# Kernel optimization log

Measured on AMD Instinct MI355X. Metric: run time of the kernel, lower is better.

The kernel has to match this reference:

```python
import jax, jax.numpy as jnp
import numpy as np

C = 256
EPS = 1e-5

def layer_norm(x, g, b):
    mu = jnp.mean(x, axis=-1, keepdims=True)
    var = jnp.var(x, axis=-1, keepdims=True)
    return (x - mu) * jax.lax.rsqrt(var + EPS) * g + b

def setup_inputs() -> dict:
    key = jax.random.key(0)
    ks = jax.random.split(key, 12)
    B, H, W = 1, 64, 64
    s = 1.0 / np.sqrt(C)
    inp = {
        'lidar_features': jax.random.normal(ks[0], (B, C, H, W), jnp.float32),
        'image_features': jax.random.normal(ks[1], (B, C, H, W), jnp.float32),
        'Wq': jax.random.normal(ks[2], (C, C), jnp.float32) * s,
        'bq': jnp.zeros((C,), jnp.float32),
        'Wk': jax.random.normal(ks[3], (C, C), jnp.float32) * s,
        'bk': jnp.zeros((C,), jnp.float32),
        'Wv': jax.random.normal(ks[4], (C, C), jnp.float32) * s,
        'bv': jnp.zeros((C,), jnp.float32),
        'Wo': jax.random.normal(ks[5], (C, C), jnp.float32) * s,
        'bo': jnp.zeros((C,), jnp.float32),
        'g1': jnp.ones((C,), jnp.float32),
        'b1': jnp.zeros((C,), jnp.float32),
        'W1': jax.random.normal(ks[6], (C, 4 * C), jnp.float32) * s,
        'bf1': jnp.zeros((4 * C,), jnp.float32),
        'W2': jax.random.normal(ks[7], (4 * C, C), jnp.float32) * (1.0 / np.sqrt(4 * C)),
        'bf2': jnp.zeros((C,), jnp.float32),
        'g2': jnp.ones((C,), jnp.float32),
        'b2': jnp.zeros((C,), jnp.float32),
        'num_heads': 8,
    }
    return inp

def reference(lidar_features, image_features, Wq, bq, Wk, bk, Wv, bv, Wo, bo,
              g1, b1, W1, bf1, W2, bf2, g2, b2, num_heads):
    B, Cc, H, W = lidar_features.shape
    S = H * W
    hd = Cc // num_heads
    # [B,C,H,W] -> [B,S,C]
    x = lidar_features.reshape(B, Cc, S).transpose(0, 2, 1)
    y = image_features.reshape(B, Cc, S).transpose(0, 2, 1)
    q = x @ Wq + bq            # [B,S,C]
    k = y @ Wk + bk
    v = y @ Wv + bv
    qh = q.reshape(B, S, num_heads, hd).transpose(0, 2, 1, 3)  # [B,h,S,d]
    kh = k.reshape(B, S, num_heads, hd).transpose(0, 2, 1, 3)
    vh = v.reshape(B, S, num_heads, hd).transpose(0, 2, 1, 3)
    attn = jnp.einsum('bhqd,bhkd->bhqk', qh, kh) / jnp.sqrt(jnp.float32(hd))
    attn = jax.nn.softmax(attn, axis=-1)
    out = jnp.einsum('bhqk,bhkd->bhqd', attn, vh)
    out = out.transpose(0, 2, 1, 3).reshape(B, S, Cc)
    out = out @ Wo + bo
    # residual is the projected q in [B,S,C] layout (intended semantics)
    out = layer_norm(q + out, g1, b1)
    ffn = jax.nn.relu(out @ W1 + bf1) @ W2 + bf2
    out = layer_norm(out + ffn, g2, b2)
    return out.reshape(B, H, W, Cc).transpose(0, 3, 1, 2)
```

## Files before the change

### kernel.cpp

```cpp
#include <hip/hip_runtime.h>

#define SQ 4096
#define CCH 256
#define NH 8
#define HD 32
#define LN_EPS 1e-5f
#define NSPLIT 8

typedef __bf16 bf16x8 __attribute__((ext_vector_type(8)));
typedef float f32x4 __attribute__((ext_vector_type(4)));
using bf16 = __bf16;

#define LOG2E 1.4426950408889634f

__device__ __forceinline__ void tile_tc(const float* __restrict__ src, bf16* __restrict__ dst,
                                        int R, int Ccol, int ti, int tj) {
    __shared__ float t[32][33];
    const int tx = threadIdx.x & 31;
    const int ty = threadIdx.x >> 5;
    const int i0 = ti * 32, j0 = tj * 32;
    #pragma unroll
    for (int i = 0; i < 32; i += 8)
        t[ty + i][tx] = src[(size_t)(i0 + ty + i) * Ccol + j0 + tx];
    __syncthreads();
    #pragma unroll
    for (int i = 0; i < 32; i += 8)
        dst[(size_t)(j0 + ty + i) * R + i0 + tx] = (bf16)t[tx][ty + i];
}

__global__ __launch_bounds__(256)
void cvt_inputs(const float* __restrict__ x, const float* __restrict__ y,
                bf16* __restrict__ xT, bf16* __restrict__ yT) {
    const float* s = blockIdx.z ? y : x;
    bf16* d = blockIdx.z ? yT : xT;
    tile_tc(s, d, CCH, SQ, blockIdx.y, blockIdx.x);
}

__global__ __launch_bounds__(256)
void cvt_weights(const float* Wq, const float* Wk, const float* Wv, const float* Wo,
                 const float* W1, const float* W2,
                 bf16* WqT, bf16* WkT, bf16* WvT, bf16* WoT, bf16* W1T, bf16* W2T) {
    const int id = blockIdx.x;
    if (id < 256) {
        const int w = id >> 6, local = id & 63;
        const float* s = (w == 0) ? Wq : (w == 1) ? Wk : (w == 2) ? Wv : Wo;
        bf16* d = (w == 0) ? WqT : (w == 1) ? WkT : (w == 2) ? WvT : WoT;
        tile_tc(s, d, 256, 256, local >> 3, local & 7);
    } else if (id < 512) {
        const int local = id - 256;
        tile_tc(W1, W1T, 256, 1024, local >> 5, local & 31);
    } else {
        const int local = id - 512;
        tile_tc(W2, W2T, 1024, 256, local >> 3, local & 7);
    }
}

template <int K, int OUT_MODE, bool RELU>
__global__ __launch_bounds__(256)
void gemm_mfma(const bf16* __restrict__ A, const bf16* __restrict__ BT,
               const float* __restrict__ bias, float* __restrict__ Cf,
               bf16* __restrict__ Cb, int N, float bscale) {
    const int tid = threadIdx.x;
    const int w = tid >> 6, l = tid & 63;
    const int l15 = l & 15, lg = l >> 4;
    const int m0 = blockIdx.x * 64 + (w >> 1) * 32;
    const int n0 = blockIdx.y * 64 + (w & 1) * 32;

    f32x4 acc[2][2] = {};
    const bf16* a0 = &A[(size_t)(m0 + l15) * K + lg * 8];
    const bf16* b0 = &BT[(size_t)(n0 + l15) * K + lg * 8];

    for (int k0 = 0; k0 < K; k0 += 32) {
        bf16x8 a[2], b[2];
        a[0] = *reinterpret_cast<const bf16x8*>(a0 + k0);
        a[1] = *reinterpret_cast<const bf16x8*>(a0 + (size_t)16 * K + k0);
        b[0] = *reinterpret_cast<const bf16x8*>(b0 + k0);
        b[1] = *reinterpret_cast<const bf16x8*>(b0 + (size_t)16 * K + k0);
        #pragma unroll
        for (int i = 0; i < 2; ++i)
            #pragma unroll
            for (int j = 0; j < 2; ++j)
                acc[i][j] = __builtin_amdgcn_mfma_f32_16x16x32_bf16(a[i], b[j], acc[i][j], 0, 0, 0);
    }

    #pragma unroll
    for (int i = 0; i < 2; ++i) {
        #pragma unroll
        for (int j = 0; j < 2; ++j) {
            const int col = n0 + j * 16 + l15;
            const float bs = bias[col];
            #pragma unroll
            for (int r = 0; r < 4; ++r) {
                const int row = m0 + i * 16 + lg * 4 + r;
                float val = acc[i][j][r] + bs;
                if (RELU) val = fmaxf(val, 0.f);
                if constexpr (OUT_MODE == 0)
                    Cf[(size_t)row * N + col] = val;
                if constexpr (OUT_MODE == 2)
                    Cb[(size_t)row * N + col] = (bf16)(val * bscale);
            }
        }
    }
}

__global__ __launch_bounds__(256)
void qkv_gemm(const bf16* __restrict__ xT, const bf16* __restrict__ yT,
              const bf16* __restrict__ WqT, const bf16* __restrict__ WkT,
              const bf16* __restrict__ WvT,
              const float* __restrict__ bq, const float* __restrict__ bk,
              const float* __restrict__ bv,
              bf16* __restrict__ qb, bf16* __restrict__ kbb, bf16* __restrict__ vTb,
              float kscale) {
    const int z = blockIdx.z;
    const bf16* A  = (z == 0) ? xT : yT;
    const bf16* BT = (z == 0) ? WqT : (z == 1) ? WkT : WvT;
    const float* bias = (z == 0) ? bq : (z == 1) ? bk : bv;

    const int tid = threadIdx.x;
    const int w = tid >> 6, l = tid & 63;
    const int l15 = l & 15, lg = l >> 4;
    const int m0 = blockIdx.x * 64 + (w >> 1) * 32;
    const int n0 = blockIdx.y * 64 + (w & 1) * 32;

    f32x4 acc[2][2] = {};
    const bf16* a0 = &A[(size_t)(m0 + l15) * CCH + lg * 8];
    const bf16* b0 = &BT[(size_t)(n0 + l15) * CCH + lg * 8];

    for (int k0 = 0; k0 < CCH; k0 += 32) {
        bf16x8 a[2], b[2];
        a[0] = *reinterpret_cast<const bf16x8*>(a0 + k0);
        a[1] = *reinterpret_cast<const bf16x8*>(a0 + (size_t)16 * CCH + k0);
        b[0] = *reinterpret_cast<const bf16x8*>(b0 + k0);
        b[1] = *reinterpret_cast<const bf16x8*>(b0 + (size_t)16 * CCH + k0);
        #pragma unroll
        for (int i = 0; i < 2; ++i)
            #pragma unroll
            for (int j = 0; j < 2; ++j)
                acc[i][j] = __builtin_amdgcn_mfma_f32_16x16x32_bf16(a[i], b[j], acc[i][j], 0, 0, 0);
    }

    const float sc = (z == 1) ? kscale : 1.f;
    #pragma unroll
    for (int i = 0; i < 2; ++i) {
        #pragma unroll
        for (int j = 0; j < 2; ++j) {
            const int col = n0 + j * 16 + l15;
            const float bs = bias[col];
            #pragma unroll
            for (int r = 0; r < 4; ++r) {
                const int row = m0 + i * 16 + lg * 4 + r;
                float val = acc[i][j][r] + bs;
                if (z == 2)
                    vTb[(size_t)col * SQ + row] = (bf16)val;
                else if (z == 1)
                    kbb[(size_t)row * CCH + col] = (bf16)(val * sc);
                else
                    qb[(size_t)row * CCH + col] = (bf16)val;
            }
        }
    }
}

__global__ __launch_bounds__(256)
void flash_attn9(const bf16* __restrict__ qb, const bf16* __restrict__ kb,
                 const bf16* __restrict__ vT, bf16* __restrict__ Op,
                 float* __restrict__ Lp) {
    const int fid = blockIdx.x + 16 * (blockIdx.y + NH * blockIdx.z);
    const int nid = (fid & 7) * 128 + (fid >> 3);
    const int q0 = (nid & 15) * 256;
    const int h  = (nid >> 4) & 7;
    const int sp = nid >> 7;

    const int tid = threadIdx.x;
    const int w = tid >> 6, l = tid & 63;
    const int l15 = l & 15, lg = l >> 4;

    __shared__ unsigned int Sb[4][2][8][72];

    bf16x8 aq[4];
    #pragma unroll
    for (int su = 0; su < 4; ++su)
        aq[su] = *reinterpret_cast<const bf16x8*>(
            &qb[(size_t)(q0 + su * 64 + w * 16 + l15) * CCH + h * HD + lg * 8]);

    float lac[4] = {0.f, 0.f, 0.f, 0.f};
    f32x4 o[4][2] = {};

    const bf16* kfrag = &kb[(size_t)l15 * CCH + h * HD + lg * 8];
    const bf16* vfrag = &vT[(size_t)(h * HD + l15) * SQ + lg * 8];

    const int kt0 = sp * (SQ / NSPLIT / 64);
    const int kt1 = kt0 + (SQ / NSPLIT / 64);

    for (int kt = kt0; kt < kt1; ++kt) {
        const int kb0 = kt * 64;

        bf16x8 kf[4], vf[2][2];
        #pragma unroll
        for (int t = 0; t < 4; ++t)
            kf[t] = *reinterpret_cast<const bf16x8*>(kfrag + (size_t)(kb0 + t * 16) * CCH);
        #pragma unroll
        for (int dh = 0; dh < 2; ++dh)
            #pragma unroll
            for (int kh = 0; kh < 2; ++kh)
                vf[dh][kh] = *reinterpret_cast<const bf16x8*>(
                    vfrag + (size_t)dh * 16 * SQ + kb0 + kh * 32);

        #pragma unroll
        for (int su = 0; su < 4; ++su) {
            const int par = su & 1;
            f32x4 s[4];
            #pragma unroll
            for (int t = 0; t < 4; ++t)
                s[t] = __builtin_amdgcn_mfma_f32_16x16x32_bf16(
                    kf[t], aq[su], (f32x4){0.f, 0.f, 0.f, 0.f}, 0, 0, 0);

            #pragma unroll
            for (int t = 0; t < 4; ++t) {
                float p0 = exp2f(s[t][0]), p1 = exp2f(s[t][1]);
                float p2 = exp2f(s[t][2]), p3 = exp2f(s[t][3]);
                lac[su] += (p0 + p1) + (p2 + p3);
                unsigned int u0 = __builtin_bit_cast(unsigned int, p0) + 0x8000u;
                unsigned int u1 = __builtin_bit_cast(unsigned int, p1) + 0x8000u;
                unsigned int u2 = __builtin_bit_cast(unsigned int, p2) + 0x8000u;
                unsigned int u3 = __builtin_bit_cast(unsigned int, p3) + 0x8000u;
                Sb[w][par][t * 2 + 0][l] = __builtin_amdgcn_perm(u1, u0, 0x07060302u);
                Sb[w][par][t * 2 + 1][l] = __builtin_amdgcn_perm(u3, u2, 0x07060302u);
            }

            #pragma unroll
            for (int kh = 0; kh < 2; ++kh) {
                const int sbase = kh * 4 + (lg >> 1) * 2;
                const int i0 = l15 + 16 * ((lg & 1) * 2);
                const int i1 = i0 + 16;
                union { unsigned int u[4]; bf16x8 v; } pb;
                pb.u[0] = Sb[w][par][sbase + 0][i0];
                pb.u[1] = Sb[w][par][sbase + 1][i0];
                pb.u[2] = Sb[w][par][sbase + 0][i1];
                pb.u[3] = Sb[w][par][sbase + 1][i1];
                #pragma unroll
                for (int dh = 0; dh < 2; ++dh)
                    o[su][dh] = __builtin_amdgcn_mfma_f32_16x16x32_bf16(
                        vf[dh][kh], pb.v, o[su][dh], 0, 0, 0);
            }
        }
    }

    const size_t obase = ((size_t)sp * NH + h) * HD;
    #pragma unroll
    for (int su = 0; su < 4; ++su) {
        float lx = lac[su];
        lx += __shfl_xor(lx, 16);
        lx += __shfl_xor(lx, 32);
        const int qrow = q0 + su * 64 + w * 16 + l15;
        #pragma unroll
        for (int dh = 0; dh < 2; ++dh)
            #pragma unroll
            for (int r = 0; r < 4; ++r)
                Op[(obase + dh * 16 + lg * 4 + r) * SQ + qrow] = (bf16)o[su][dh][r];
        if (lg == 0)
            Lp[((size_t)sp * NH + h) * SQ + qrow] = lx;
    }
}

__global__ __launch_bounds__(256)
void attn_merge3(const bf16* __restrict__ Op, const float* __restrict__ Lp,
                 bf16* __restrict__ atb) {
    const int h = blockIdx.y;
    const int q0 = blockIdx.x * 64;
    const int t = threadIdx.x;
    __shared__ float sInv[64];
    __shared__ float trans[32][65];

    if (t < 64) {
        float L = 0.f;
        #pragma unroll
        for (int sp = 0; sp < NSPLIT; ++sp)
            L += Lp[((size_t)sp * NH + h) * SQ + q0 + t];
        sInv[t] = 1.0f / L;
    }
    __syncthreads();

    const int q = t & 63, dg = t >> 6;
    float a[8] = {0.f, 0.f, 0.f, 0.f, 0.f, 0.f, 0.f, 0.f};
    for (int sp = 0; sp < NSPLIT; ++sp) {
        const size_t rb = ((size_t)sp * NH + h) * HD;
        #pragma unroll
        for (int i = 0; i < 8; ++i) {
            const int d = i * 4 + dg;
            a[i] += (float)Op[(rb + d) * SQ + q0 + q];
        }
    }
    const float invq = sInv[q];
    #pragma unroll
    for (int i = 0; i < 8; ++i)
        trans[i * 4 + dg][q] = a[i] * invq;
    __syncthreads();

    const int oq = t >> 2, od = (t & 3) * 8;
    bf16x8 o8;
    #pragma unroll
    for (int j = 0; j < 8; ++j) o8[j] = (bf16)trans[od + j][oq];
    *reinterpret_cast<bf16x8*>(&atb[(size_t)(q0 + oq) * CCH + h * HD + od]) = o8;
}

__global__ __launch_bounds__(256)
void add_ln1(const bf16* __restrict__ a, const float* __restrict__ b,
             const float* __restrict__ g, const float* __restrict__ beta,
             float* __restrict__ out, bf16* __restrict__ outb) {
    const int s = blockIdx.x;
    const int c = threadIdx.x;
    float val = (float)a[(size_t)s * CCH + c] + b[(size_t)s * CCH + c];
    float sum = val, sq = val * val;
    #pragma unroll
    for (int off = 1; off < 64; off <<= 1) {
        sum += __shfl_xor(sum, off);
        sq  += __shfl_xor(sq, off);
    }
    __shared__ float ssum[4], ssq[4];
    int w = c >> 6;
    if ((c & 63) == 0) { ssum[w] = sum; ssq[w] = sq; }
    __syncthreads();
    sum = ssum[0] + ssum[1] + ssum[2] + ssum[3];
    sq  = ssq[0] + ssq[1] + ssq[2] + ssq[3];
    float mu = sum * (1.0f / CCH);
    float var = sq * (1.0f / CCH) - mu * mu;
    float rs = rsqrtf(var + LN_EPS);
    float res = (val - mu) * rs * g[c] + beta[c];
    out[(size_t)s * CCH + c] = res;
    outb[(size_t)s * CCH + c] = (bf16)res;
}

__global__ __launch_bounds__(256)
void add_ln_t(const float* __restrict__ a, const float* __restrict__ b,
              const float* __restrict__ g, const float* __restrict__ beta,
              float* __restrict__ out) {
    const int s0 = blockIdx.x * 32;
    const int t = threadIdx.x;
    const int row = t >> 3;
    const int e8 = t & 7;
    const size_t base = (size_t)(s0 + row) * CCH + e8 * 32;

    float v[32];
    float sum = 0.f, sq = 0.f;
    #pragma unroll
    for (int j = 0; j < 32; j += 4) {
        float4 va = *reinterpret_cast<const float4*>(&a[base + j]);
        float4 vb = *reinterpret_cast<const float4*>(&b[base + j]);
        v[j]     = va.x + vb.x;
        v[j + 1] = va.y + vb.y;
        v[j + 2] = va.z + vb.z;
        v[j + 3] = va.w + vb.w;
        sum += (v[j] + v[j + 1]) + (v[j + 2] + v[j + 3]);
        sq  += (v[j] * v[j] + v[j + 1] * v[j + 1]) + (v[j + 2] * v[j + 2] + v[j + 3] * v[j + 3]);
    }
    sum += __shfl_xor(sum, 1); sum += __shfl_xor(sum, 2); sum += __shfl_xor(sum, 4);
    sq  += __shfl_xor(sq, 1);  sq  += __shfl_xor(sq, 2);  sq  += __shfl_xor(sq, 4);
    const float mu = sum * (1.0f / CCH);
    const float var = sq * (1.0f / CCH) - mu * mu;
    const float rs = rsqrtf(var + LN_EPS);
    #pragma unroll
    for (int j = 0; j < 32; j += 4) {
        float4 gg = *reinterpret_cast<const float4*>(&g[e8 * 32 + j]);
        float4 bb = *reinterpret_cast<const float4*>(&beta[e8 * 32 + j]);
        v[j]     = (v[j]     - mu) * rs * gg.x + bb.x;
        v[j + 1] = (v[j + 1] - mu) * rs * gg.y + bb.y;
        v[j + 2] = (v[j + 2] - mu) * rs * gg.z + bb.z;
        v[j + 3] = (v[j + 3] - mu) * rs * gg.w + bb.w;
    }

    __shared__ float tile[32][33];
    const int cl = t >> 3, f4 = (t & 7) * 4;
    for (int c = 0; c < 8; ++c) {
        __syncthreads();
        if (e8 == c) {
            #pragma unroll
            for (int j = 0; j < 32; ++j) tile[j][row] = v[j];
        }
        __syncthreads();
        float4 o4 = {tile[cl][f4], tile[cl][f4 + 1], tile[cl][f4 + 2], tile[cl][f4 + 3]};
        *reinterpret_cast<float4*>(&out[(size_t)(c * 32 + cl) * SQ + s0 + f4]) = o4;
    }
}

extern "C" void kernel_launch(void* const* d_in, const int* in_sizes, int n_in,
                              void* d_out, int out_size, void* d_ws, size_t ws_size,
                              hipStream_t stream) {
    const float* lidar = (const float*)d_in[0];
    const float* image = (const float*)d_in[1];
    const float* Wq  = (const float*)d_in[2];
    const float* bq  = (const float*)d_in[3];
    const float* Wk  = (const float*)d_in[4];
    const float* bk  = (const float*)d_in[5];
    const float* Wv  = (const float*)d_in[6];
    const float* bv  = (const float*)d_in[7];
    const float* Wo  = (const float*)d_in[8];
    const float* bo  = (const float*)d_in[9];
    const float* g1  = (const float*)d_in[10];
    const float* b1  = (const float*)d_in[11];
    const float* W1  = (const float*)d_in[12];
    const float* bf1 = (const float*)d_in[13];
    const float* W2  = (const float*)d_in[14];
    const float* bf2 = (const float*)d_in[15];
    const float* g2  = (const float*)d_in[16];
    const float* b2  = (const float*)d_in[17];
    float* out = (float*)d_out;

    char* ws = (char*)d_ws;
    const size_t KB = 1024, MBy = 1024 * 1024;
    bf16* qb   = (bf16*)(ws + 0);
    bf16* kbb  = (bf16*)(ws + 2 * MBy);
    bf16* vTb  = (bf16*)(ws + 4 * MBy);
    bf16* WoT  = (bf16*)(ws + 6 * MBy);
    bf16* W1T  = (bf16*)(ws + 6 * MBy + 128 * KB);
    bf16* W2T  = (bf16*)(ws + 6 * MBy + 640 * KB);
    bf16* WqT  = (bf16*)(ws + 6 * MBy + 1152 * KB);
    bf16* WkT  = (bf16*)(ws + 6 * MBy + 1280 * KB);
    bf16* WvT  = (bf16*)(ws + 6 * MBy + 1408 * KB);
    bf16* xT   = (bf16*)(ws + 7 * MBy + 512 * KB);
    bf16* yT   = (bf16*)(ws + 9 * MBy + 512 * KB);
    bf16* Op   = (bf16*)(ws + 7 * MBy + 512 * KB);
    float* Lp  = (float*)d_out;
    bf16* atb  = (bf16*)(ws + 2 * MBy);
    float* o   = (float*)(ws + 7 * MBy + 512 * KB);
    float* ln1 = (float*)(ws + 11 * MBy + 512 * KB);
    bf16* ln1b = (bf16*)(ws + 4 * MBy);
    bf16* h1   = (bf16*)(ws + 15 * MBy + 512 * KB);
    float* h2  = (float*)(ws + 7 * MBy + 512 * KB);

    const float qscale = 0.17677669529663687f * 1.4426950408889634f;
    dim3 blk(256);

    cvt_inputs<<<dim3(SQ / 32, CCH / 32, 2), blk, 0, stream>>>(lidar, image, xT, yT);
    cvt_weights<<<dim3(768), blk, 0, stream>>>(Wq, Wk, Wv, Wo, W1, W2,
                                               WqT, WkT, WvT, WoT, W1T, W2T);
    qkv_gemm<<<dim3(64, 4, 3), blk, 0, stream>>>(xT, yT, WqT, WkT, WvT,
                                                 bq, bk, bv, qb, kbb, vTb, qscale);
    flash_attn9<<<dim3(SQ / 256, NH, NSPLIT), blk, 0, stream>>>(qb, kbb, vTb, Op, Lp);
    attn_merge3<<<dim3(SQ / 64, NH), blk, 0, stream>>>(Op, Lp, atb);
    gemm_mfma<256, 0, false><<<dim3(64, 4), blk, 0, stream>>>(atb, WoT, bo, o, nullptr, 256, 1.f);
    add_ln1<<<SQ, blk, 0, stream>>>(qb, o, g1, b1, ln1, ln1b);
    gemm_mfma<256, 2, true ><<<dim3(64, 16), blk, 0, stream>>>(ln1b, W1T, bf1, nullptr, h1, 1024, 1.f);
    gemm_mfma<1024, 0, false><<<dim3(64, 4), blk, 0, stream>>>(h1, W2T, bf2, h2, nullptr, 256, 1.f);
    add_ln_t<<<dim3(SQ / 32), blk, 0, stream>>>(ln1, h2, g2, b2, out);
}
```

Baseline: 141.3 us.

## Compute softmax row sums via ones-row MFMA, halve attention splits, split-K output GEMMs

The V-transpose buffer is padded with 16 extra rows per head, one of them all ones, so an extra MFMA yields the softmax denominator and replaces the scalar per-lane sum accumulation. Rounding before bf16 packing is dropped. Attention KV splits drop from 8 to 4, giving longer loops per block and fewer partials to merge. The Wo and W2 GEMMs become split-K with two partial outputs that the layernorm kernels add together, which doubles block count for these small GEMMs at the cost of extra memory traffic. The workspace layout is reshuffled to fit the larger buffers.

```diff
diff --git a/kernel.cpp b/kernel.cpp
--- a/kernel.cpp
+++ b/kernel.cpp
@@ -5,13 +5,12 @@
 #define NH 8
 #define HD 32
 #define LN_EPS 1e-5f
-#define NSPLIT 8
+#define NSPLIT 4
+#define VROWS 48
 
 typedef __bf16 bf16x8 __attribute__((ext_vector_type(8)));
 typedef float f32x4 __attribute__((ext_vector_type(4)));
 using bf16 = __bf16;
-
-#define LOG2E 1.4426950408889634f
 
 __device__ __forceinline__ void tile_tc(const float* __restrict__ src, bf16* __restrict__ dst,
                                         int R, int Ccol, int ti, int tj) {
@@ -39,7 +38,8 @@
 __global__ __launch_bounds__(256)
 void cvt_weights(const float* Wq, const float* Wk, const float* Wv, const float* Wo,
                  const float* W1, const float* W2,
-                 bf16* WqT, bf16* WkT, bf16* WvT, bf16* WoT, bf16* W1T, bf16* W2T) {
+                 bf16* WqT, bf16* WkT, bf16* WvT, bf16* WoT, bf16* W1T, bf16* W2T,
+                 bf16* vTb) {
     const int id = blockIdx.x;
     if (id < 256) {
         const int w = id >> 6, local = id & 63;
@@ -49,9 +49,23 @@
     } else if (id < 512) {
         const int local = id - 256;
         tile_tc(W1, W1T, 256, 1024, local >> 5, local & 31);
-    } else {
+    } else if (id < 768) {
         const int local = id - 512;
         tile_tc(W2, W2T, 1024, 256, local >> 3, local & 7);
+    } else {
+        const int local = id - 768;
+        #pragma unroll
+        for (int rr = 0; rr < 2; ++rr) {
+            const int pr = local * 2 + rr;
+            const int hh = pr >> 4, j = pr & 15;
+            const bf16 val = (bf16)((j == 0) ? 1.0f : 0.0f);
+            bf16x8 v8;
+            #pragma unroll
+            for (int e = 0; e < 8; ++e) v8[e] = val;
+            bf16* dst = vTb + ((size_t)hh * VROWS + 32 + j) * SQ + threadIdx.x * 16;
+            *reinterpret_cast<bf16x8*>(dst) = v8;
+            *reinterpret_cast<bf16x8*>(dst + 8) = v8;
+        }
     }
 }
 
@@ -59,7 +73,7 @@
 __global__ __launch_bounds__(256)
 void gemm_mfma(const bf16* __restrict__ A, const bf16* __restrict__ BT,
                const float* __restrict__ bias, float* __restrict__ Cf,
-               bf16* __restrict__ Cb, int N, float bscale) {
+               bf16* __restrict__ Cb, int N) {
     const int tid = threadIdx.x;
     const int w = tid >> 6, l = tid & 63;
     const int l15 = l & 15, lg = l >> 4;
@@ -97,7 +111,52 @@
                 if constexpr (OUT_MODE == 0)
                     Cf[(size_t)row * N + col] = val;
                 if constexpr (OUT_MODE == 2)
-                    Cb[(size_t)row * N + col] = (bf16)(val * bscale);
+                    Cb[(size_t)row * N + col] = (bf16)val;
+            }
+        }
+    }
+}
+
+template <int K, int KS>
+__global__ __launch_bounds__(256)
+void gemm_sk(const bf16* __restrict__ A, const bf16* __restrict__ BT,
+             const float* __restrict__ bias, float* __restrict__ Cf, int N) {
+    constexpr int KSL = K / KS;
+    const int z = blockIdx.z;
+    const int tid = threadIdx.x;
+    const int w = tid >> 6, l = tid & 63;
+    const int l15 = l & 15, lg = l >> 4;
+    const int m0 = blockIdx.x * 64 + (w >> 1) * 32;
+    const int n0 = blockIdx.y * 64 + (w & 1) * 32;
+
+    f32x4 acc[2][2] = {};
+    const bf16* a0 = &A[(size_t)(m0 + l15) * K + z * KSL + lg * 8];
+    const bf16* b0 = &BT[(size_t)(n0 + l15) * K + z * KSL + lg * 8];
+
+    for (int k0 = 0; k0 < KSL; k0 += 32) {
+        bf16x8 a[2], b[2];
+        a[0] = *reinterpret_cast<const bf16x8*>(a0 + k0);
+        a[1] = *reinterpret_cast<const bf16x8*>(a0 + (size_t)16 * K + k0);
+        b[0] = *reinterpret_cast<const bf16x8*>(b0 + k0);
+        b[1] = *reinterpret_cast<const bf16x8*>(b0 + (size_t)16 * K + k0);
+        #pragma unroll
+        for (int i = 0; i < 2; ++i)
+            #pragma unroll
+            for (int j = 0; j < 2; ++j)
+                acc[i][j] = __builtin_amdgcn_mfma_f32_16x16x32_bf16(a[i], b[j], acc[i][j], 0, 0, 0);
+    }
+
+    float* C = Cf + (size_t)z * SQ * N;
+    #pragma unroll
+    for (int i = 0; i < 2; ++i) {
+        #pragma unroll
+        for (int j = 0; j < 2; ++j) {
+            const int col = n0 + j * 16 + l15;
+            const float bs = (z == 0) ? bias[col] : 0.f;
+            #pragma unroll
+            for (int r = 0; r < 4; ++r) {
+                const int row = m0 + i * 16 + lg * 4 + r;
+                C[(size_t)row * N + col] = acc[i][j][r] + bs;
             }
         }
     }
@@ -151,7 +210,7 @@
                 const int row = m0 + i * 16 + lg * 4 + r;
                 float val = acc[i][j][r] + bs;
                 if (z == 2)
-                    vTb[(size_t)col * SQ + row] = (bf16)val;
+                    vTb[((size_t)(col >> 5) * VROWS + (col & 31)) * SQ + row] = (bf16)val;
                 else if (z == 1)
                     kbb[(size_t)row * CCH + col] = (bf16)(val * sc);
                 else
@@ -162,11 +221,11 @@
 }
 
 __global__ __launch_bounds__(256)
-void flash_attn9(const bf16* __restrict__ qb, const bf16* __restrict__ kb,
-                 const bf16* __restrict__ vT, bf16* __restrict__ Op,
-                 float* __restrict__ Lp) {
+void flash_attn10(const bf16* __restrict__ qb, const bf16* __restrict__ kb,
+                  const bf16* __restrict__ vT, bf16* __restrict__ Op,
+                  float* __restrict__ Lp) {
     const int fid = blockIdx.x + 16 * (blockIdx.y + NH * blockIdx.z);
-    const int nid = (fid & 7) * 128 + (fid >> 3);
+    const int nid = (fid & 7) * 64 + (fid >> 3);
     const int q0 = (nid & 15) * 256;
     const int h  = (nid >> 4) & 7;
     const int sp = nid >> 7;
@@ -183,11 +242,11 @@
         aq[su] = *reinterpret_cast<const bf16x8*>(
             &qb[(size_t)(q0 + su * 64 + w * 16 + l15) * CCH + h * HD + lg * 8]);
 
-    float lac[4] = {0.f, 0.f, 0.f, 0.f};
     f32x4 o[4][2] = {};
+    f32x4 o2[4] = {};
 
     const bf16* kfrag = &kb[(size_t)l15 * CCH + h * HD + lg * 8];
-    const bf16* vfrag = &vT[(size_t)(h * HD + l15) * SQ + lg * 8];
+    const bf16* vfrag = &vT[((size_t)h * VROWS + l15) * SQ + lg * 8];
 
     const int kt0 = sp * (SQ / NSPLIT / 64);
     const int kt1 = kt0 + (SQ / NSPLIT / 64);
@@ -195,12 +254,12 @@
     for (int kt = kt0; kt < kt1; ++kt) {
         const int kb0 = kt * 64;
 
-        bf16x8 kf[4], vf[2][2];
+        bf16x8 kf[4], vf[3][2];
         #pragma unroll
         for (int t = 0; t < 4; ++t)
             kf[t] = *reinterpret_cast<const bf16x8*>(kfrag + (size_t)(kb0 + t * 16) * CCH);
         #pragma unroll
-        for (int dh = 0; dh < 2; ++dh)
+        for (int dh = 0; dh < 3; ++dh)
             #pragma unroll
             for (int kh = 0; kh < 2; ++kh)
                 vf[dh][kh] = *reinterpret_cast<const bf16x8*>(
@@ -217,13 +276,10 @@
 
             #pragma unroll
             for (int t = 0; t < 4; ++t) {
-                float p0 = exp2f(s[t][0]), p1 = exp2f(s[t][1]);
-                float p2 = exp2f(s[t][2]), p3 = exp2f(s[t][3]);
-                lac[su] += (p0 + p1) + (p2 + p3);
-                unsigned int u0 = __builtin_bit_cast(unsigned int, p0) + 0x8000u;
-                unsigned int u1 = __builtin_bit_cast(unsigned int, p1) + 0x8000u;
-                unsigned int u2 = __builtin_bit_cast(unsigned int, p2) + 0x8000u;
-                unsigned int u3 = __builtin_bit_cast(unsigned int, p3) + 0x8000u;
+                unsigned int u0 = __builtin_bit_cast(unsigned int, exp2f(s[t][0]));
+                unsigned int u1 = __builtin_bit_cast(unsigned int, exp2f(s[t][1]));
+                unsigned int u2 = __builtin_bit_cast(unsigned int, exp2f(s[t][2]));
+                unsigned int u3 = __builtin_bit_cast(unsigned int, exp2f(s[t][3]));
                 Sb[w][par][t * 2 + 0][l] = __builtin_amdgcn_perm(u1, u0, 0x07060302u);
                 Sb[w][par][t * 2 + 1][l] = __builtin_amdgcn_perm(u3, u2, 0x07060302u);
             }
@@ -242,6 +298,8 @@
                 for (int dh = 0; dh < 2; ++dh)
                     o[su][dh] = __builtin_amdgcn_mfma_f32_16x16x32_bf16(
                         vf[dh][kh], pb.v, o[su][dh], 0, 0, 0);
+                o2[su] = __builtin_amdgcn_mfma_f32_16x16x32_bf16(
+                    vf[2][kh], pb.v, o2[su], 0, 0, 0);
             }
         }
     }
@@ -249,9 +307,6 @@
     const size_t obase = ((size_t)sp * NH + h) * HD;
     #pragma unroll
     for (int su = 0; su < 4; ++su) {
-        float lx = lac[su];
-        lx += __shfl_xor(lx, 16);
-        lx += __shfl_xor(lx, 32);
         const int qrow = q0 + su * 64 + w * 16 + l15;
         #pragma unroll
         for (int dh = 0; dh < 2; ++dh)
@@ -259,7 +314,7 @@
             for (int r = 0; r < 4; ++r)
                 Op[(obase + dh * 16 + lg * 4 + r) * SQ + qrow] = (bf16)o[su][dh][r];
         if (lg == 0)
-            Lp[((size_t)sp * NH + h) * SQ + qrow] = lx;
+            Lp[((size_t)sp * NH + h) * SQ + qrow] = o2[su][0];
     }
 }
 
@@ -310,7 +365,8 @@
              float* __restrict__ out, bf16* __restrict__ outb) {
     const int s = blockIdx.x;
     const int c = threadIdx.x;
-    float val = (float)a[(size_t)s * CCH + c] + b[(size_t)s * CCH + c];
+    const size_t idx = (size_t)s * CCH + c;
+    float val = (float)a[idx] + b[idx] + b[idx + (size_t)SQ * CCH];
     float sum = val, sq = val * val;
     #pragma unroll
     for (int off = 1; off < 64; off <<= 1) {
@@ -327,8 +383,8 @@
     float var = sq * (1.0f / CCH) - mu * mu;
     float rs = rsqrtf(var + LN_EPS);
     float res = (val - mu) * rs * g[c] + beta[c];
-    out[(size_t)s * CCH + c] = res;
-    outb[(size_t)s * CCH + c] = (bf16)res;
+    out[idx] = res;
+    outb[idx] = (bf16)res;
 }
 
 __global__ __launch_bounds__(256)
@@ -340,6 +396,7 @@
     const int row = t >> 3;
     const int e8 = t & 7;
     const size_t base = (size_t)(s0 + row) * CCH + e8 * 32;
+    const size_t PS = (size_t)SQ * CCH;
 
     float v[32];
     float sum = 0.f, sq = 0.f;
@@ -347,10 +404,11 @@
     for (int j = 0; j < 32; j += 4) {
         float4 va = *reinterpret_cast<const float4*>(&a[base + j]);
         float4 vb = *reinterpret_cast<const float4*>(&b[base + j]);
-        v[j]     = va.x + vb.x;
-        v[j + 1] = va.y + vb.y;
-        v[j + 2] = va.z + vb.z;
-        v[j + 3] = va.w + vb.w;
+        float4 vc = *reinterpret_cast<const float4*>(&b[base + PS + j]);
+        v[j]     = va.x + vb.x + vc.x;
+        v[j + 1] = va.y + vb.y + vc.y;
+        v[j + 2] = va.z + vb.z + vc.z;
+        v[j + 3] = va.w + vb.w + vc.w;
         sum += (v[j] + v[j + 1]) + (v[j + 2] + v[j + 3]);
         sq  += (v[j] * v[j] + v[j + 1] * v[j + 1]) + (v[j + 2] * v[j + 2] + v[j + 3] * v[j + 3]);
     }
@@ -407,40 +465,40 @@
     float* out = (float*)d_out;
 
     char* ws = (char*)d_ws;
-    const size_t KB = 1024, MBy = 1024 * 1024;
-    bf16* qb   = (bf16*)(ws + 0);
-    bf16* kbb  = (bf16*)(ws + 2 * MBy);
-    bf16* vTb  = (bf16*)(ws + 4 * MBy);
-    bf16* WoT  = (bf16*)(ws + 6 * MBy);
-    bf16* W1T  = (bf16*)(ws + 6 * MBy + 128 * KB);
-    bf16* W2T  = (bf16*)(ws + 6 * MBy + 640 * KB);
-    bf16* WqT  = (bf16*)(ws + 6 * MBy + 1152 * KB);
-    bf16* WkT  = (bf16*)(ws + 6 * MBy + 1280 * KB);
-    bf16* WvT  = (bf16*)(ws + 6 * MBy + 1408 * KB);
-    bf16* xT   = (bf16*)(ws + 7 * MBy + 512 * KB);
-    bf16* yT   = (bf16*)(ws + 9 * MBy + 512 * KB);
-    bf16* Op   = (bf16*)(ws + 7 * MBy + 512 * KB);
-    float* Lp  = (float*)d_out;
-    bf16* atb  = (bf16*)(ws + 2 * MBy);
-    float* o   = (float*)(ws + 7 * MBy + 512 * KB);
-    float* ln1 = (float*)(ws + 11 * MBy + 512 * KB);
-    bf16* ln1b = (bf16*)(ws + 4 * MBy);
-    bf16* h1   = (bf16*)(ws + 15 * MBy + 512 * KB);
-    float* h2  = (float*)(ws + 7 * MBy + 512 * KB);
+    const size_t KB = 1024;
+    bf16* W2T = (bf16*)(ws + 0);
+    bf16* W1T = (bf16*)(ws + 512 * KB);
+    bf16* WoT = (bf16*)(ws + 1024 * KB);
+    bf16* WqT = (bf16*)(ws + 1152 * KB);
+    bf16* WkT = (bf16*)(ws + 1280 * KB);
+    bf16* WvT = (bf16*)(ws + 1408 * KB);
+    bf16* qb  = (bf16*)(ws + 1536 * KB);
+    bf16* kbb = (bf16*)(ws + 3584 * KB);
+    bf16* vTb = (bf16*)(ws + 5632 * KB);
+    bf16* xT  = (bf16*)(ws + 8704 * KB);
+    bf16* yT  = (bf16*)(ws + 10752 * KB);
+    bf16* Op  = (bf16*)(ws + 8704 * KB);
+    float* Lp = (float*)d_out;
+    bf16* atb = (bf16*)(ws + 3584 * KB);
+    float* o01 = (float*)(ws + 8704 * KB);
+    float* ln1 = (float*)(ws + 19968 * KB);
+    bf16* ln1b = (bf16*)(ws + 5632 * KB);
+    bf16* h1  = (bf16*)(ws + 9728 * KB);
+    float* h2 = (float*)(ws + 1536 * KB);
 
     const float qscale = 0.17677669529663687f * 1.4426950408889634f;
     dim3 blk(256);
 
     cvt_inputs<<<dim3(SQ / 32, CCH / 32, 2), blk, 0, stream>>>(lidar, image, xT, yT);
-    cvt_weights<<<dim3(768), blk, 0, stream>>>(Wq, Wk, Wv, Wo, W1, W2,
-                                               WqT, WkT, WvT, WoT, W1T, W2T);
+    cvt_weights<<<dim3(832), blk, 0, stream>>>(Wq, Wk, Wv, Wo, W1, W2,
+                                               WqT, WkT, WvT, WoT, W1T, W2T, vTb);
     qkv_gemm<<<dim3(64, 4, 3), blk, 0, stream>>>(xT, yT, WqT, WkT, WvT,
                                                  bq, bk, bv, qb, kbb, vTb, qscale);
-    flash_attn9<<<dim3(SQ / 256, NH, NSPLIT), blk, 0, stream>>>(qb, kbb, vTb, Op, Lp);
+    flash_attn10<<<dim3(SQ / 256, NH, NSPLIT), blk, 0, stream>>>(qb, kbb, vTb, Op, Lp);
     attn_merge3<<<dim3(SQ / 64, NH), blk, 0, stream>>>(Op, Lp, atb);
-    gemm_mfma<256, 0, false><<<dim3(64, 4), blk, 0, stream>>>(atb, WoT, bo, o, nullptr, 256, 1.f);
-    add_ln1<<<SQ, blk, 0, stream>>>(qb, o, g1, b1, ln1, ln1b);
-    gemm_mfma<256, 2, true ><<<dim3(64, 16), blk, 0, stream>>>(ln1b, W1T, bf1, nullptr, h1, 1024, 1.f);
-    gemm_mfma<1024, 0, false><<<dim3(64, 4), blk, 0, stream>>>(h1, W2T, bf2, h2, nullptr, 256, 1.f);
+    gemm_sk<256, 2><<<dim3(64, 4, 2), blk, 0, stream>>>(atb, WoT, bo, o01, 256);
+    add_ln1<<<SQ, blk, 0, stream>>>(qb, o01, g1, b1, ln1, ln1b);
+    gemm_mfma<256, 2, true><<<dim3(64, 16), blk, 0, stream>>>(ln1b, W1T, bf1, nullptr, h1, 1024);
+    gemm_sk<1024, 2><<<dim3(64, 4, 2), blk, 0, stream>>>(h1, W2T, bf2, h2, 256);
     add_ln_t<<<dim3(SQ / 32), blk, 0, stream>>>(ln1, h2, g2, b2, out);
 }
```

Measured after the change: 143.5 us. Within noise of the previous version (+1.6%).
